# Performance work log

Measured on AMD Instinct MI355X. Metric: run time of the kernel, lower is better.

## Reference

```python
import jax, jax.numpy as jnp
import numpy as np

ALPHA = 100.0
MARGIN = 5


def _weight_mask(bb, H, W):
    """Analytic per-pixel weight for one sample. bb: (4,2) int, cols = (x, y)."""
    m = MARGIN
    y_min, y_max = bb[:, 1].min(), bb[:, 1].max()
    x_min, x_max = bb[:, 0].min(), bb[:, 0].max()
    ys = jnp.arange(H)[:, None]   # (H,1)
    xs = jnp.arange(W)[None, :]   # (1,W)

    inside = (ys >= y_min) & (ys < y_max) & (xs >= x_min) & (xs < x_max)
    w = jnp.where(inside, ALPHA, 1.0)

    # border region is only weighted when bbox+margin is strictly interior
    cond = (x_min - m > 0) & (x_max + m < W) & (y_min - m > 0) & (y_max + m < H)

    # vertical ramp factor: m inside bbox rows, 1..m on top strip, m..1 on bottom strip, 0 outside
    fy = jnp.where((ys >= y_min) & (ys < y_max), m,
         jnp.where((ys >= y_min - m) & (ys < y_min), ys - (y_min - m) + 1,
         jnp.where((ys >= y_max) & (ys < y_max + m), m - (ys - y_max), 0)))
    fx = jnp.where((xs >= x_min) & (xs < x_max), m,
         jnp.where((xs >= x_min - m) & (xs < x_min), xs - (x_min - m) + 1,
         jnp.where((xs >= x_max) & (xs < x_max + m), m - (xs - x_max), 0)))

    band = (fy > 0) & (fx > 0) & (~inside)
    # linear policy: strips use their own ramp, corners use min of the two ramps
    lin = jnp.minimum(fy, fx).astype(w.dtype) / m * ALPHA
    w = jnp.where(cond & band, lin, w)
    return w  # (H, W)


def setup_inputs() -> dict:
    key = jax.random.key(0)
    k1, k2, k3 = jax.random.split(key, 3)
    B, C, H, W = 32, 3, 512, 512
    x = jax.random.normal(k1, (B, C, H, W), dtype=jnp.float32)
    y = jax.random.normal(k2, (B, C, H, W), dtype=jnp.float32)
    bbox = jax.random.randint(k3, (B, 4, 2), 0, 512, dtype=jnp.int32)
    return {"x": x, "y": y, "bbox": bbox}


def reference(x, y, bbox):
    B, C, H, W = x.shape
    w = jax.vmap(lambda bb: _weight_mask(bb, H, W))(bbox)  # (B,H,W)
    return jnp.mean(jnp.abs(x - y) * w[:, None, :, :])
```

## Files before the change

### kernel.cpp

```cpp
#include <hip/hip_runtime.h>

#define HW_PLANE (512 * 512)
#define QUADS_PER_BATCH (HW_PLANE / 4)
#define BLOCKS_PER_BATCH 64
#define QUADS_PER_BLOCK (QUADS_PER_BATCH / BLOCKS_PER_BATCH)
#define NBLOCKS (32 * BLOCKS_PER_BATCH)
#define N_ELEMS (32 * 3 * HW_PLANE)

__global__ __launch_bounds__(256) void mae_bbox_kernel(
    const float* __restrict__ x, const float* __restrict__ y,
    const int* __restrict__ bbox, float* __restrict__ ws) {

    const int b     = blockIdx.x >> 6;
    const int chunk = blockIdx.x & 63;

    const int* bb = bbox + (b << 3);
    const int xmin = min(min(bb[0], bb[2]), min(bb[4], bb[6]));
    const int xmax = max(max(bb[0], bb[2]), max(bb[4], bb[6]));
    const int ymin = min(min(bb[1], bb[3]), min(bb[5], bb[7]));
    const int ymax = max(max(bb[1], bb[3]), max(bb[5], bb[7]));
    const bool cond = (xmin > 5) && (xmax < 507) && (ymin > 5) && (ymax < 507);

    const size_t bbase = (size_t)(b * 3) * HW_PLANE;
    float acc = 0.0f;

#pragma unroll
    for (int it = 0; it < 4; ++it) {
        const int qb = chunk * QUADS_PER_BLOCK + it * 256 + (int)threadIdx.x;
        const int p  = qb << 2;
        const int h  = p >> 9;
        const int w0 = p & 511;

        const bool inrow = (h >= ymin) && (h < ymax);
        const int fy = inrow ? 5
                     : ((h >= ymin - 5 && h < ymin) ? (h - ymin + 6)
                     : ((h >= ymax && h < ymax + 5) ? (5 - (h - ymax)) : 0));

        float wq[4];
#pragma unroll
        for (int j = 0; j < 4; ++j) {
            const int wx = w0 + j;
            const bool incol = (wx >= xmin) && (wx < xmax);
            const int fx = incol ? 5
                         : ((wx >= xmin - 5 && wx < xmin) ? (wx - xmin + 6)
                         : ((wx >= xmax && wx < xmax + 5) ? (5 - (wx - xmax)) : 0));
            const bool inside = inrow && incol;
            float wv = inside ? 100.0f : 1.0f;
            if (cond && (fy > 0) && (fx > 0) && !inside)
                wv = (float)min(fy, fx) * 20.0f;
            wq[j] = wv;
        }

        const size_t base = bbase + (size_t)p;
#pragma unroll
        for (int c = 0; c < 3; ++c) {
            const float4 xv = *reinterpret_cast<const float4*>(x + base + (size_t)c * HW_PLANE);
            const float4 yv = *reinterpret_cast<const float4*>(y + base + (size_t)c * HW_PLANE);
            acc = fmaf(fabsf(xv.x - yv.x), wq[0], acc);
            acc = fmaf(fabsf(xv.y - yv.y), wq[1], acc);
            acc = fmaf(fabsf(xv.z - yv.z), wq[2], acc);
            acc = fmaf(fabsf(xv.w - yv.w), wq[3], acc);
        }
    }

#pragma unroll
    for (int off = 32; off > 0; off >>= 1) acc += __shfl_down(acc, off, 64);

    __shared__ float sred[4];
    const int lane = threadIdx.x & 63;
    const int wid  = threadIdx.x >> 6;
    if (lane == 0) sred[wid] = acc;
    __syncthreads();
    if (threadIdx.x == 0)
        ws[blockIdx.x] = sred[0] + sred[1] + sred[2] + sred[3];
}

__global__ __launch_bounds__(256) void finalize_kernel(
    const float* __restrict__ ws, float* __restrict__ out) {
    float acc = 0.0f;
#pragma unroll
    for (int i = 0; i < NBLOCKS / 256; ++i)
        acc += ws[i * 256 + threadIdx.x];

#pragma unroll
    for (int off = 32; off > 0; off >>= 1) acc += __shfl_down(acc, off, 64);

    __shared__ float sred[4];
    const int lane = threadIdx.x & 63;
    const int wid  = threadIdx.x >> 6;
    if (lane == 0) sred[wid] = acc;
    __syncthreads();
    if (threadIdx.x == 0)
        out[0] = (sred[0] + sred[1] + sred[2] + sred[3]) * (1.0f / (float)N_ELEMS);
}

extern "C" void kernel_launch(void* const* d_in, const int* in_sizes, int n_in,
                              void* d_out, int out_size, void* d_ws, size_t ws_size,
                              hipStream_t stream) {
    const float* x    = (const float*)d_in[0];
    const float* y    = (const float*)d_in[1];
    const int*   bbox = (const int*)d_in[2];
    float* out = (float*)d_out;
    float* ws  = (float*)d_ws;

    mae_bbox_kernel<<<NBLOCKS, 256, 0, stream>>>(x, y, bbox, ws);
    finalize_kernel<<<1, 256, 0, stream>>>(ws, out);
}
```

Measured before the change: 213.7 us.

## Split grid per channel and batch all loads up front per thread

Work is now split over a 3D grid of (chunk, channel, batch), so each block handles one channel plane chunk instead of looping over all three channels. Each thread issues all eight float4 loads of x and y before any arithmetic, which raises memory-level parallelism. Column weights are hoisted out of the row loop. Per-pixel weight computation is now repeated for each channel (three times more ALU work for weights), and register pressure rises from holding 16 float4 values.

```diff
diff --git a/kernel.cpp b/kernel.cpp
--- a/kernel.cpp
+++ b/kernel.cpp
@@ -1,18 +1,17 @@
 #include <hip/hip_runtime.h>
 
 #define HW_PLANE (512 * 512)
-#define QUADS_PER_BATCH (HW_PLANE / 4)
-#define BLOCKS_PER_BATCH 64
-#define QUADS_PER_BLOCK (QUADS_PER_BATCH / BLOCKS_PER_BATCH)
-#define NBLOCKS (32 * BLOCKS_PER_BATCH)
 #define N_ELEMS (32 * 3 * HW_PLANE)
+#define NBLOCKS (96 * 32)
 
 __global__ __launch_bounds__(256) void mae_bbox_kernel(
     const float* __restrict__ x, const float* __restrict__ y,
     const int* __restrict__ bbox, float* __restrict__ ws) {
 
-    const int b     = blockIdx.x >> 6;
-    const int chunk = blockIdx.x & 63;
+    const int chunk = blockIdx.x;
+    const int c     = blockIdx.y;
+    const int b     = blockIdx.z;
+    const int tid   = threadIdx.x;
 
     const int* bb = bbox + (b << 3);
     const int xmin = min(min(bb[0], bb[2]), min(bb[4], bb[6]));
@@ -21,16 +20,34 @@
     const int ymax = max(max(bb[1], bb[3]), max(bb[5], bb[7]));
     const bool cond = (xmin > 5) && (xmax < 507) && (ymin > 5) && (ymax < 507);
 
-    const size_t bbase = (size_t)(b * 3) * HW_PLANE;
+    const size_t base = ((size_t)(b * 3 + c) << 18) + ((size_t)chunk << 13) + (size_t)(tid << 2);
+
+    float4 xv[8], yv[8];
+#pragma unroll
+    for (int k = 0; k < 8; ++k)
+        xv[k] = *reinterpret_cast<const float4*>(x + base + (size_t)(k << 10));
+#pragma unroll
+    for (int k = 0; k < 8; ++k)
+        yv[k] = *reinterpret_cast<const float4*>(y + base + (size_t)(k << 10));
+
+    const int w0     = (tid << 2) & 511;
+    const int h_base = (chunk << 4) + (tid >> 7);
+
+    int   fx[4];
+    bool  incol[4];
+#pragma unroll
+    for (int j = 0; j < 4; ++j) {
+        const int wx = w0 + j;
+        incol[j] = (wx >= xmin) && (wx < xmax);
+        fx[j] = incol[j] ? 5
+              : ((wx >= xmin - 5 && wx < xmin) ? (wx - xmin + 6)
+              : ((wx >= xmax && wx < xmax + 5) ? (5 - (wx - xmax)) : 0));
+    }
+
     float acc = 0.0f;
-
 #pragma unroll
-    for (int it = 0; it < 4; ++it) {
-        const int qb = chunk * QUADS_PER_BLOCK + it * 256 + (int)threadIdx.x;
-        const int p  = qb << 2;
-        const int h  = p >> 9;
-        const int w0 = p & 511;
-
+    for (int k = 0; k < 8; ++k) {
+        const int h = h_base + (k << 1);
         const bool inrow = (h >= ymin) && (h < ymax);
         const int fy = inrow ? 5
                      : ((h >= ymin - 5 && h < ymin) ? (h - ymin + 6)
@@ -39,40 +56,31 @@
         float wq[4];
 #pragma unroll
         for (int j = 0; j < 4; ++j) {
-            const int wx = w0 + j;
-            const bool incol = (wx >= xmin) && (wx < xmax);
-            const int fx = incol ? 5
-                         : ((wx >= xmin - 5 && wx < xmin) ? (wx - xmin + 6)
-                         : ((wx >= xmax && wx < xmax + 5) ? (5 - (wx - xmax)) : 0));
-            const bool inside = inrow && incol;
+            const bool inside = inrow && incol[j];
             float wv = inside ? 100.0f : 1.0f;
-            if (cond && (fy > 0) && (fx > 0) && !inside)
-                wv = (float)min(fy, fx) * 20.0f;
+            if (cond && (fy > 0) && (fx[j] > 0) && !inside)
+                wv = (float)min(fy, fx[j]) * 20.0f;
             wq[j] = wv;
         }
 
-        const size_t base = bbase + (size_t)p;
-#pragma unroll
-        for (int c = 0; c < 3; ++c) {
-            const float4 xv = *reinterpret_cast<const float4*>(x + base + (size_t)c * HW_PLANE);
-            const float4 yv = *reinterpret_cast<const float4*>(y + base + (size_t)c * HW_PLANE);
-            acc = fmaf(fabsf(xv.x - yv.x), wq[0], acc);
-            acc = fmaf(fabsf(xv.y - yv.y), wq[1], acc);
-            acc = fmaf(fabsf(xv.z - yv.z), wq[2], acc);
-            acc = fmaf(fabsf(xv.w - yv.w), wq[3], acc);
-        }
+        acc = fmaf(fabsf(xv[k].x - yv[k].x), wq[0], acc);
+        acc = fmaf(fabsf(xv[k].y - yv[k].y), wq[1], acc);
+        acc = fmaf(fabsf(xv[k].z - yv[k].z), wq[2], acc);
+        acc = fmaf(fabsf(xv[k].w - yv[k].w), wq[3], acc);
     }
 
 #pragma unroll
     for (int off = 32; off > 0; off >>= 1) acc += __shfl_down(acc, off, 64);
 
     __shared__ float sred[4];
-    const int lane = threadIdx.x & 63;
-    const int wid  = threadIdx.x >> 6;
+    const int lane = tid & 63;
+    const int wid  = tid >> 6;
     if (lane == 0) sred[wid] = acc;
     __syncthreads();
-    if (threadIdx.x == 0)
-        ws[blockIdx.x] = sred[0] + sred[1] + sred[2] + sred[3];
+    if (tid == 0) {
+        const int bid = ((b * 3 + c) << 5) + chunk;
+        ws[bid] = sred[0] + sred[1] + sred[2] + sred[3];
+    }
 }
 
 __global__ __launch_bounds__(256) void finalize_kernel(
@@ -103,6 +111,7 @@
     float* out = (float*)d_out;
     float* ws  = (float*)d_ws;
 
-    mae_bbox_kernel<<<NBLOCKS, 256, 0, stream>>>(x, y, bbox, ws);
+    dim3 grid(32, 3, 32);
+    mae_bbox_kernel<<<grid, 256, 0, stream>>>(x, y, bbox, ws);
     finalize_kernel<<<1, 256, 0, stream>>>(ws, out);
 }
```

Result: no change. 214.0 us (+0.1%).
